# Performance work log

Measured on AMD Instinct MI355X. Metric: run time of the kernel, lower is better.

## Reference

```python
import jax, jax.numpy as jnp
import numpy as np


def setup_inputs() -> dict:
    key = jax.random.key(0)
    k1, k2 = jax.random.split(key)
    B, T, D = 16, 4096, 512
    x = jax.random.normal(k1, (B, T, D), dtype=jnp.float32)
    alpha = jax.random.normal(k2, (1, 1, D), dtype=jnp.float32)  # raw param, pre-sigmoid
    return {"x": x, "alpha": alpha}


def reference(x, alpha):
    # s_0 = x_0 ; s_t = a * x_t + (1 - a) * s_{t-1}, a = sigmoid(alpha)
    a = jax.nn.sigmoid(alpha[0, 0, :])  # (D,)
    one_minus_a = 1.0 - a

    def step(prev, xt):  # prev, xt: (B, D)
        cur = a * xt + one_minus_a * prev
        return cur, cur

    x_t = jnp.swapaxes(x, 0, 1)  # (T, B, D)
    init = x_t[0]
    _, rest = jax.lax.scan(step, init, x_t[1:])  # (T-1, B, D)
    states = jnp.concatenate([x_t[:1], rest], axis=0)  # (T, B, D)
    return jnp.swapaxes(states, 0, 1)  # (B, T, D)
```

## Files before the change

### kernel.cpp

```cpp
#include <hip/hip_runtime.h>
#include <math.h>

#define BB 16
#define TT 4096
#define DD 512
#define D4 128
#define CC 128
#define LL 32
#define NBY 8

#define FLAGS_OFF_U32 64
#define ENDS_OFF_B    8192

typedef float v4f __attribute__((ext_vector_type(4)));

__device__ __forceinline__ float sigmf(float v) {
    return 1.0f / (1.0f + expf(-v));
}

__device__ __forceinline__ void nt_store4(float4* p, const float4& s) {
    __builtin_nontemporal_store(*reinterpret_cast<const v4f*>(&s),
                                reinterpret_cast<v4f*>(p));
}

__global__ __launch_bounds__(256) void es_single(
    const float* __restrict__ x, const float* __restrict__ alpha,
    unsigned int* __restrict__ hdr, float* __restrict__ out)
{
    const int tid = threadIdx.x;

    __shared__ unsigned int tkt_s;
    if (tid == 0) tkt_s = atomicAdd(hdr, 1u);
    __syncthreads();
    const unsigned int t = tkt_s;
    const int by = (int)(t & (NBY - 1));
    const int c  = (int)(t >> 3);

    const int b  = (by << 1) + (tid >> 7);
    const int d4 = tid & 127;

    unsigned int* flags = hdr + FLAGS_OFF_U32;
    float4* ends = reinterpret_cast<float4*>(reinterpret_cast<char*>(hdr) + ENDS_OFF_B);

    const float4 al = reinterpret_cast<const float4*>(alpha)[d4];
    const float ax = sigmf(al.x), ay = sigmf(al.y), az = sigmf(al.z), aw = sigmf(al.w);
    const float fx = 1.0f - ax, fy = 1.0f - ay, fz = 1.0f - az, fw = 1.0f - aw;

    const size_t base = ((size_t)b * TT + (size_t)c * LL) * D4 + d4;
    const float4* xp = reinterpret_cast<const float4*>(x) + base;
    float4*       op = reinterpret_cast<float4*>(out) + base;

    float4 buf[LL];
    #pragma unroll
    for (int i = 0; i < LL; ++i) buf[i] = xp[(size_t)i * D4];

    float4 s;
    if (c == 0) { s = buf[0]; }
    else        { s.x = s.y = s.z = s.w = 0.0f; }
    #pragma unroll
    for (int i = 0; i < LL; ++i) {
        s.x = fmaf(ax, buf[i].x, fx * s.x);
        s.y = fmaf(ay, buf[i].y, fy * s.y);
        s.z = fmaf(az, buf[i].z, fz * s.z);
        s.w = fmaf(aw, buf[i].w, fw * s.w);
    }
    ends[((size_t)b * CC + c) * D4 + d4] = s;

    __syncthreads();
    if (tid == 0) {
        __hip_atomic_store(&flags[(by << 7) + c], 1u,
                           __ATOMIC_RELEASE, __HIP_MEMORY_SCOPE_AGENT);
    }

    float4 S;
    if (c > 0) {
        if (tid < c) {
            while (__hip_atomic_load(&flags[(by << 7) + tid],
                                     __ATOMIC_RELAXED, __HIP_MEMORY_SCOPE_AGENT) == 0u) {
                __builtin_amdgcn_s_sleep(2);
            }
        }
        __syncthreads();
        __builtin_amdgcn_fence(__ATOMIC_ACQUIRE, "agent");

        float4 fL;
        fL.x = powf(fx, (float)LL);
        fL.y = powf(fy, (float)LL);
        fL.z = powf(fz, (float)LL);
        fL.w = powf(fw, (float)LL);

        const float4* e = ends + (size_t)b * CC * D4 + d4;
        S = e[0];
        int j = 1;
        for (; j + 4 <= c; j += 4) {
            float4 v0 = e[(size_t)(j + 0) * D4];
            float4 v1 = e[(size_t)(j + 1) * D4];
            float4 v2 = e[(size_t)(j + 2) * D4];
            float4 v3 = e[(size_t)(j + 3) * D4];
            S.x = fmaf(fL.x, S.x, v0.x); S.y = fmaf(fL.y, S.y, v0.y);
            S.z = fmaf(fL.z, S.z, v0.z); S.w = fmaf(fL.w, S.w, v0.w);
            S.x = fmaf(fL.x, S.x, v1.x); S.y = fmaf(fL.y, S.y, v1.y);
            S.z = fmaf(fL.z, S.z, v1.z); S.w = fmaf(fL.w, S.w, v1.w);
            S.x = fmaf(fL.x, S.x, v2.x); S.y = fmaf(fL.y, S.y, v2.y);
            S.z = fmaf(fL.z, S.z, v2.z); S.w = fmaf(fL.w, S.w, v2.w);
            S.x = fmaf(fL.x, S.x, v3.x); S.y = fmaf(fL.y, S.y, v3.y);
            S.z = fmaf(fL.z, S.z, v3.z); S.w = fmaf(fL.w, S.w, v3.w);
        }
        for (; j < c; ++j) {
            const float4 v = e[(size_t)j * D4];
            S.x = fmaf(fL.x, S.x, v.x);
            S.y = fmaf(fL.y, S.y, v.y);
            S.z = fmaf(fL.z, S.z, v.z);
            S.w = fmaf(fL.w, S.w, v.w);
        }
    }

    float4 sf;
    if (c == 0) sf = buf[0];
    else        sf = S;
    #pragma unroll
    for (int i = 0; i < LL; ++i) {
        sf.x = fmaf(ax, buf[i].x, fx * sf.x);
        sf.y = fmaf(ay, buf[i].y, fy * sf.y);
        sf.z = fmaf(az, buf[i].z, fz * sf.z);
        sf.w = fmaf(aw, buf[i].w, fw * sf.w);
        nt_store4(op + (size_t)i * D4, sf);
    }
}

__global__ __launch_bounds__(256) void es_serial(
    const float* __restrict__ x, const float* __restrict__ alpha,
    float* __restrict__ out)
{
    const int g  = blockIdx.x * 256 + threadIdx.x;
    const int b  = g >> 7;
    const int d4 = g & 127;

    const float4 al = reinterpret_cast<const float4*>(alpha)[d4];
    const float ax = sigmf(al.x), ay = sigmf(al.y), az = sigmf(al.z), aw = sigmf(al.w);
    const float fx = 1.0f - ax, fy = 1.0f - ay, fz = 1.0f - az, fw = 1.0f - aw;

    const float4* xp = reinterpret_cast<const float4*>(x) + (size_t)b * TT * D4 + d4;
    float4*       op = reinterpret_cast<float4*>(out) + (size_t)b * TT * D4 + d4;

    float4 s = xp[0];
    #pragma unroll 4
    for (int t = 0; t < TT; ++t) {
        const float4 v = xp[(size_t)t * D4];
        s.x = fmaf(ax, v.x, fx * s.x);
        s.y = fmaf(ay, v.y, fy * s.y);
        s.z = fmaf(az, v.z, fz * s.z);
        s.w = fmaf(aw, v.w, fw * s.w);
        op[(size_t)t * D4] = s;
    }
}

extern "C" void kernel_launch(void* const* d_in, const int* in_sizes, int n_in,
                              void* d_out, int out_size, void* d_ws, size_t ws_size,
                              hipStream_t stream)
{
    const float* x     = (const float*)d_in[0];
    const float* alpha = (const float*)d_in[1];
    float*       out   = (float*)d_out;

    const size_t need = (size_t)ENDS_OFF_B + (size_t)BB * CC * DD * sizeof(float);
    if (ws_size < need) {
        es_serial<<<dim3(8), 256, 0, stream>>>(x, alpha, out);
        return;
    }

    hipMemsetAsync(d_ws, 0, ENDS_OFF_B, stream);

    es_single<<<dim3(CC * NBY), 256, 0, stream>>>(
        x, alpha, (unsigned int*)d_ws, out);
}
```

Measured before the change: 322.0 us.

## Stage chunks in LDS via async global-to-LDS loads and split time across half-blocks

Each block now handles one batch row and one 32-step chunk. The chunk is loaded into 64 KB of LDS with global_load_lds instead of a 32-deep register buffer. The two half-blocks each compute 16 timesteps, and the second half derives its start state by combining its local partial with the carry-in times (1-a)^16. This cuts register pressure and per-thread serial length and doubles the grid. In exchange it uses large dynamic LDS, which limits occupancy, and it doubles the number of flag-chained blocks, so carry resolution across more blocks costs more.

New measurement: 378.1 us. +17.4%, slower.

```diff
diff --git a/kernel.cpp b/kernel.cpp
--- a/kernel.cpp
+++ b/kernel.cpp
@@ -7,12 +7,15 @@
 #define D4 128
 #define CC 128
 #define LL 32
-#define NBY 8
+#define LH 16
+#define TILE_B 65536
 
 #define FLAGS_OFF_U32 64
-#define ENDS_OFF_B    8192
+#define ENDS_OFF_B    16384
 
 typedef float v4f __attribute__((ext_vector_type(4)));
+typedef const __attribute__((address_space(1))) unsigned int gua_t;
+typedef __attribute__((address_space(3))) unsigned int lua_t;
 
 __device__ __forceinline__ float sigmf(float v) {
     return 1.0f / (1.0f + expf(-v));
@@ -23,71 +26,98 @@
                                 reinterpret_cast<v4f*>(p));
 }
 
-__global__ __launch_bounds__(256) void es_single(
+__device__ __forceinline__ void gload_lds16(const void* g, void* l) {
+    __builtin_amdgcn_global_load_lds((gua_t*)g, (lua_t*)l, 16, 0, 0);
+}
+
+__global__ __launch_bounds__(256) void es_fused(
     const float* __restrict__ x, const float* __restrict__ alpha,
     unsigned int* __restrict__ hdr, float* __restrict__ out)
 {
-    const int tid = threadIdx.x;
-
-    __shared__ unsigned int tkt_s;
-    if (tid == 0) tkt_s = atomicAdd(hdr, 1u);
-    __syncthreads();
-    const unsigned int t = tkt_s;
-    const int by = (int)(t & (NBY - 1));
-    const int c  = (int)(t >> 3);
-
-    const int b  = (by << 1) + (tid >> 7);
+    extern __shared__ char smem[];
+    const int tid  = threadIdx.x;
+    const int wave = tid >> 6;
+    const int lane = tid & 63;
+
+    if (tid == 0) *((unsigned int*)smem) = atomicAdd(hdr, 1u);
+    __syncthreads();
+    const unsigned int tk = *((const unsigned int*)smem);
+    __syncthreads();
+
+    const int b = (int)(tk & (BB - 1));
+    const int c = (int)(tk >> 4);
+
+    const int th = tid >> 7;
     const int d4 = tid & 127;
 
     unsigned int* flags = hdr + FLAGS_OFF_U32;
     float4* ends = reinterpret_cast<float4*>(reinterpret_cast<char*>(hdr) + ENDS_OFF_B);
+
+    {
+        const char* gbase = (const char*)x
+                          + ((size_t)b * TT + (size_t)c * LL) * (DD * sizeof(float));
+        #pragma unroll
+        for (int k = 0; k < 16; ++k) {
+            const int seg = (wave << 4) + k;
+            gload_lds16(gbase + (size_t)seg * 1024 + (size_t)lane * 16,
+                        smem + (size_t)seg * 1024);
+        }
+    }
 
     const float4 al = reinterpret_cast<const float4*>(alpha)[d4];
     const float ax = sigmf(al.x), ay = sigmf(al.y), az = sigmf(al.z), aw = sigmf(al.w);
     const float fx = 1.0f - ax, fy = 1.0f - ay, fz = 1.0f - az, fw = 1.0f - aw;
-
-    const size_t base = ((size_t)b * TT + (size_t)c * LL) * D4 + d4;
-    const float4* xp = reinterpret_cast<const float4*>(x) + base;
-    float4*       op = reinterpret_cast<float4*>(out) + base;
-
-    float4 buf[LL];
+    float4 fL, fH;
+    fL.x = powf(fx, (float)LL); fL.y = powf(fy, (float)LL);
+    fL.z = powf(fz, (float)LL); fL.w = powf(fw, (float)LL);
+    fH.x = powf(fx, (float)LH); fH.y = powf(fy, (float)LH);
+    fH.z = powf(fz, (float)LH); fH.w = powf(fw, (float)LH);
+
+    __syncthreads();
+
+    const char* sbase = smem + (size_t)d4 * 16;
+    #define LDS_AT(tt) (*reinterpret_cast<const float4*>(sbase + (size_t)(tt) * 2048))
+
+    float4 sE;
+    if (c == 0) { sE = LDS_AT(0); }
+    else        { sE.x = sE.y = sE.z = sE.w = 0.0f; }
     #pragma unroll
-    for (int i = 0; i < LL; ++i) buf[i] = xp[(size_t)i * D4];
-
-    float4 s;
-    if (c == 0) { s = buf[0]; }
-    else        { s.x = s.y = s.z = s.w = 0.0f; }
-    #pragma unroll
-    for (int i = 0; i < LL; ++i) {
-        s.x = fmaf(ax, buf[i].x, fx * s.x);
-        s.y = fmaf(ay, buf[i].y, fy * s.y);
-        s.z = fmaf(az, buf[i].z, fz * s.z);
-        s.w = fmaf(aw, buf[i].w, fw * s.w);
-    }
-    ends[((size_t)b * CC + c) * D4 + d4] = s;
+    for (int i = 0; i < LH; ++i) {
+        const float4 v = LDS_AT(i);
+        sE.x = fmaf(ax, v.x, fx * sE.x);
+        sE.y = fmaf(ay, v.y, fy * sE.y);
+        sE.z = fmaf(az, v.z, fz * sE.z);
+        sE.w = fmaf(aw, v.w, fw * sE.w);
+    }
+    const float4 loE = sE;
+    if (th == 0) {
+        #pragma unroll
+        for (int i = LH; i < LL; ++i) {
+            const float4 v = LDS_AT(i);
+            sE.x = fmaf(ax, v.x, fx * sE.x);
+            sE.y = fmaf(ay, v.y, fy * sE.y);
+            sE.z = fmaf(az, v.z, fz * sE.z);
+            sE.w = fmaf(aw, v.w, fw * sE.w);
+        }
+        ends[((size_t)b * CC + c) * D4 + d4] = sE;
+    }
 
     __syncthreads();
     if (tid == 0) {
-        __hip_atomic_store(&flags[(by << 7) + c], 1u,
+        __hip_atomic_store(&flags[(b << 7) + c], 1u,
                            __ATOMIC_RELEASE, __HIP_MEMORY_SCOPE_AGENT);
     }
 
-    float4 S;
+    float4 S; S.x = S.y = S.z = S.w = 0.0f;
     if (c > 0) {
         if (tid < c) {
-            while (__hip_atomic_load(&flags[(by << 7) + tid],
+            while (__hip_atomic_load(&flags[(b << 7) + tid],
                                      __ATOMIC_RELAXED, __HIP_MEMORY_SCOPE_AGENT) == 0u) {
                 __builtin_amdgcn_s_sleep(2);
             }
         }
         __syncthreads();
         __builtin_amdgcn_fence(__ATOMIC_ACQUIRE, "agent");
-
-        float4 fL;
-        fL.x = powf(fx, (float)LL);
-        fL.y = powf(fy, (float)LL);
-        fL.z = powf(fz, (float)LL);
-        fL.w = powf(fw, (float)LL);
 
         const float4* e = ends + (size_t)b * CC * D4 + d4;
         S = e[0];
@@ -115,17 +145,31 @@
         }
     }
 
-    float4 sf;
-    if (c == 0) sf = buf[0];
-    else        sf = S;
+    float4 s;
+    if (th == 0) {
+        if (c == 0) s = LDS_AT(0); else s = S;
+    } else {
+        if (c == 0) { s = loE; }
+        else {
+            s.x = fmaf(fH.x, S.x, loE.x);
+            s.y = fmaf(fH.y, S.y, loE.y);
+            s.z = fmaf(fH.z, S.z, loE.z);
+            s.w = fmaf(fH.w, S.w, loE.w);
+        }
+    }
+    const int t0 = th * LH;
+    float4* op = reinterpret_cast<float4*>(out)
+               + ((size_t)b * TT + (size_t)c * LL + t0) * D4 + d4;
     #pragma unroll
-    for (int i = 0; i < LL; ++i) {
-        sf.x = fmaf(ax, buf[i].x, fx * sf.x);
-        sf.y = fmaf(ay, buf[i].y, fy * sf.y);
-        sf.z = fmaf(az, buf[i].z, fz * sf.z);
-        sf.w = fmaf(aw, buf[i].w, fw * sf.w);
-        nt_store4(op + (size_t)i * D4, sf);
-    }
+    for (int i = 0; i < LH; ++i) {
+        const float4 v = LDS_AT(t0 + i);
+        s.x = fmaf(ax, v.x, fx * s.x);
+        s.y = fmaf(ay, v.y, fy * s.y);
+        s.z = fmaf(az, v.z, fz * s.z);
+        s.w = fmaf(aw, v.w, fw * s.w);
+        nt_store4(op + (size_t)i * D4, s);
+    }
+    #undef LDS_AT
 }
 
 __global__ __launch_bounds__(256) void es_serial(
@@ -171,6 +215,6 @@
 
     hipMemsetAsync(d_ws, 0, ENDS_OFF_B, stream);
 
-    es_single<<<dim3(CC * NBY), 256, 0, stream>>>(
+    es_fused<<<dim3(CC * BB), 256, TILE_B, stream>>>(
         x, alpha, (unsigned int*)d_ws, out);
 }
```
